# Kernel tuning notes

Hardware: AMD Instinct MI355X
Metric: run time of the kernel (lower is better)

The kernel has to match this reference:

```python
import jax, jax.numpy as jnp
import numpy as np

B = 16          # number of point clouds in the batch
N_COARSE = 1024 # coarse points per cloud
N_FINE = 4096   # fine (skip) points per cloud
C_IN = 256
C_SKIP = 128
K = 3
EPS = 1e-16


def setup_inputs() -> dict:
    key = jax.random.key(0)
    ks = jax.random.split(key, 8)
    x = jax.random.normal(ks[0], (B * N_COARSE, C_IN), dtype=jnp.float32)
    pos = jax.random.uniform(ks[1], (B * N_COARSE, 3), dtype=jnp.float32)
    x_skip = jax.random.normal(ks[2], (B * N_FINE, C_SKIP), dtype=jnp.float32)
    pos_skip = jax.random.uniform(ks[3], (B * N_FINE, 3), dtype=jnp.float32)
    batch = jnp.repeat(jnp.arange(B, dtype=jnp.int64), N_COARSE)
    batch_skip = jnp.repeat(jnp.arange(B, dtype=jnp.int64), N_FINE)
    W1 = jax.random.normal(ks[4], (C_IN + C_SKIP, 256), dtype=jnp.float32) * (1.0 / np.sqrt(C_IN + C_SKIP))
    b1 = jnp.zeros((256,), dtype=jnp.float32)
    W2 = jax.random.normal(ks[5], (256, 256), dtype=jnp.float32) * (1.0 / np.sqrt(256))
    b2 = jnp.zeros((256,), dtype=jnp.float32)
    return {"x": x, "pos": pos, "batch": batch, "x_skip": x_skip,
            "pos_skip": pos_skip, "batch_skip": batch_skip,
            "W1": W1, "b1": b1, "W2": W2, "b2": b2}


def _knn_interpolate(x, pos, pos_skip):
    # Equal-sized clouds: reshape to [B, N, *] and do batched kNN.
    xc = x.reshape(B, N_COARSE, C_IN)
    pc = pos.reshape(B, N_COARSE, 3)
    pf = pos_skip.reshape(B, N_FINE, 3)
    # squared pairwise distances [B, M, N]
    d2 = (jnp.sum(pf * pf, -1)[:, :, None]
          + jnp.sum(pc * pc, -1)[:, None, :]
          - 2.0 * jnp.einsum('bmd,bnd->bmn', pf, pc))
    d2 = jnp.maximum(d2, 0.0)
    neg_d2k, idx = jax.lax.top_k(-d2, K)          # k smallest distances
    w = 1.0 / jnp.maximum(-neg_d2k, EPS)          # [B, M, K] inverse-sq-dist weights
    gathered = jax.vmap(lambda f, i: f[i])(xc, idx)  # [B, M, K, C]
    y = jnp.sum(w[..., None] * gathered, axis=2) / jnp.sum(w, axis=2, keepdims=True)
    return y.reshape(B * N_FINE, C_IN)


def reference(x, pos, batch, x_skip, pos_skip, batch_skip, W1, b1, W2, b2):
    x_interp = _knn_interpolate(x, pos, pos_skip)          # [B*M, C_IN]
    h = jnp.concatenate([x_interp, x_skip], axis=1)        # [B*M, C_IN + C_SKIP]
    h = jax.nn.relu(h @ W1 + b1)
    out = jax.nn.relu(h @ W2 + b2)
    return out
```

## Files before the change

### kernel.cpp

```cpp
#include <hip/hip_runtime.h>

typedef float  f32x4  __attribute__((ext_vector_type(4)));
typedef short  short8 __attribute__((ext_vector_type(8)));
typedef unsigned short ushort_t;
typedef ushort_t us4   __attribute__((ext_vector_type(4)));

#define NCOARSE 1024
#define NFINE   4096

__device__ __forceinline__ ushort_t f2bf(float f){
  union { float f; unsigned u; } a; a.f = f;
  unsigned u = a.u;
  return (ushort_t)((u + 0x7fffu + ((u >> 16) & 1u)) >> 16);
}

__device__ __forceinline__ f32x4 splat4(float v){ f32x4 t = {v, v, v, v}; return t; }

__global__ void prep_w(const float* __restrict__ W, ushort_t* __restrict__ Wp, int nelem){
  int e = blockIdx.x * 256 + threadIdx.x;
  if (e >= nelem) return;
  int j    = e & 7;
  int lane = (e >> 3) & 63;
  int g    = e >> 9;
  int nb   = g & 15;
  int kc   = g >> 4;
  int k = kc * 32 + (lane >> 4) * 8 + j;
  int n = nb * 16 + (lane & 15);
  Wp[e] = f2bf(W[k * 256 + n]);
}

__global__ __launch_bounds__(256) void knn_kernel(const float* __restrict__ pos,
                           const float* __restrict__ pos_skip,
                           int* __restrict__ knn_i, float* __restrict__ knn_w){
  __shared__ f32x4 cand[8][129];
  const int tid = threadIdx.x;
  const int b   = blockIdx.x >> 6;
  const int mA  = blockIdx.x * 64 + (tid >> 3);
  const int mB  = mA + 32;
  const int chunk = tid & 7;

  const float* p = pos + (size_t)b * NCOARSE * 3;
  for (int c = tid; c < NCOARSE; c += 256){
    float x = p[3*c], y = p[3*c+1], z = p[3*c+2];
    float sc = __fadd_rn(__fadd_rn(__fmul_rn(x,x), __fmul_rn(y,y)), __fmul_rn(z,z));
    f32x4 v = { x, y, z, sc };
    cand[c >> 7][c & 127] = v;
  }
  __syncthreads();

  const float* qA = pos_skip + (size_t)mA * 3;
  const float* qB = pos_skip + (size_t)mB * 3;
  float ax = qA[0], ay = qA[1], az = qA[2];
  float bx = qB[0], by = qB[1], bz = qB[2];
  float sfA = __fadd_rn(__fadd_rn(__fmul_rn(ax,ax), __fmul_rn(ay,ay)), __fmul_rn(az,az));
  float sfB = __fadd_rn(__fadd_rn(__fmul_rn(bx,bx), __fmul_rn(by,by)), __fmul_rn(bz,bz));

  float dA0 = 1e30f, dA1 = 1e30f, dA2 = 1e30f;
  int   iA0 = 0,     iA1 = 0,     iA2 = 0;
  float dB0 = 1e30f, dB1 = 1e30f, dB2 = 1e30f;
  int   iB0 = 0,     iB1 = 0,     iB2 = 0;
  const int gbase = chunk * 128;
  #pragma unroll 2
  for (int i = 0; i < 128; ++i){
    f32x4 v = cand[chunk][i];
    int gi = gbase + i;
    float dotA = __fadd_rn(__fadd_rn(__fmul_rn(ax, v.x), __fmul_rn(ay, v.y)),
                           __fmul_rn(az, v.z));
    float dA = fmaxf(__fsub_rn(__fadd_rn(sfA, v.w), __fmul_rn(2.0f, dotA)), 0.0f);
    if (dA < dA2){
      if (dA < dA1){
        dA2 = dA1; iA2 = iA1;
        if (dA < dA0){ dA1 = dA0; iA1 = iA0; dA0 = dA; iA0 = gi; }
        else         { dA1 = dA;  iA1 = gi; }
      } else { dA2 = dA; iA2 = gi; }
    }
    float dotB = __fadd_rn(__fadd_rn(__fmul_rn(bx, v.x), __fmul_rn(by, v.y)),
                           __fmul_rn(bz, v.z));
    float dB = fmaxf(__fsub_rn(__fadd_rn(sfB, v.w), __fmul_rn(2.0f, dotB)), 0.0f);
    if (dB < dB2){
      if (dB < dB1){
        dB2 = dB1; iB2 = iB1;
        if (dB < dB0){ dB1 = dB0; iB1 = iB0; dB0 = dB; iB0 = gi; }
        else         { dB1 = dB;  iB1 = gi; }
      } else { dB2 = dB; iB2 = gi; }
    }
  }

  #pragma unroll
  for (int mlev = 1; mlev <= 4; mlev <<= 1){
    float e0 = __shfl_xor(dA0, mlev), e1 = __shfl_xor(dA1, mlev), e2 = __shfl_xor(dA2, mlev);
    int   j0 = __shfl_xor(iA0, mlev), j1 = __shfl_xor(iA1, mlev), j2 = __shfl_xor(iA2, mlev);
    #pragma unroll
    for (int s = 0; s < 3; ++s){
      float e = (s == 0) ? e0 : (s == 1) ? e1 : e2;
      int   j = (s == 0) ? j0 : (s == 1) ? j1 : j2;
      bool l2 = (e < dA2) || (e == dA2 && j < iA2);
      if (l2){
        bool l1 = (e < dA1) || (e == dA1 && j < iA1);
        if (l1){
          dA2 = dA1; iA2 = iA1;
          bool l0 = (e < dA0) || (e == dA0 && j < iA0);
          if (l0){ dA1 = dA0; iA1 = iA0; dA0 = e; iA0 = j; }
          else   { dA1 = e;  iA1 = j; }
        } else { dA2 = e; iA2 = j; }
      }
    }
    float f0 = __shfl_xor(dB0, mlev), f1 = __shfl_xor(dB1, mlev), f2 = __shfl_xor(dB2, mlev);
    int   k0 = __shfl_xor(iB0, mlev), k1 = __shfl_xor(iB1, mlev), k2 = __shfl_xor(iB2, mlev);
    #pragma unroll
    for (int s = 0; s < 3; ++s){
      float e = (s == 0) ? f0 : (s == 1) ? f1 : f2;
      int   j = (s == 0) ? k0 : (s == 1) ? k1 : k2;
      bool l2 = (e < dB2) || (e == dB2 && j < iB2);
      if (l2){
        bool l1 = (e < dB1) || (e == dB1 && j < iB1);
        if (l1){
          dB2 = dB1; iB2 = iB1;
          bool l0 = (e < dB0) || (e == dB0 && j < iB0);
          if (l0){ dB1 = dB0; iB1 = iB0; dB0 = e; iB0 = j; }
          else   { dB1 = e;  iB1 = j; }
        } else { dB2 = e; iB2 = j; }
      }
    }
  }

  if (chunk == 0){
    {
      float w0 = 1.0f / fmaxf(dA0, 1e-16f);
      float w1 = 1.0f / fmaxf(dA1, 1e-16f);
      float w2 = 1.0f / fmaxf(dA2, 1e-16f);
      float ws = __fadd_rn(__fadd_rn(w0, w1), w2);
      knn_i[3*mA]   = b * NCOARSE + iA0;
      knn_i[3*mA+1] = b * NCOARSE + iA1;
      knn_i[3*mA+2] = b * NCOARSE + iA2;
      knn_w[3*mA]   = w0 / ws;
      knn_w[3*mA+1] = w1 / ws;
      knn_w[3*mA+2] = w2 / ws;
    }
    {
      float w0 = 1.0f / fmaxf(dB0, 1e-16f);
      float w1 = 1.0f / fmaxf(dB1, 1e-16f);
      float w2 = 1.0f / fmaxf(dB2, 1e-16f);
      float ws = __fadd_rn(__fadd_rn(w0, w1), w2);
      knn_i[3*mB]   = b * NCOARSE + iB0;
      knn_i[3*mB+1] = b * NCOARSE + iB1;
      knn_i[3*mB+2] = b * NCOARSE + iB2;
      knn_w[3*mB]   = w0 / ws;
      knn_w[3*mB+1] = w1 / ws;
      knn_w[3*mB+2] = w2 / ws;
    }
  }
}

#define LDW4(DST, WP, STEP)                                                   \
  { _Pragma("unroll")                                                         \
    for (int n_ = 0; n_ < 4; ++n_)                                            \
      DST[n_] = *(const short8*)((WP) +                                       \
          ((size_t)(((STEP) * 16 + wp * 4 + n_) * 64 + lane)) * 8); }

__global__ __launch_bounds__(256, 3)
void fused_fp(const float* __restrict__ x, const float* __restrict__ x_skip,
              const int* __restrict__ knn_i, const float* __restrict__ knn_w,
              const ushort_t* __restrict__ W1p, const float* __restrict__ b1,
              const ushort_t* __restrict__ W2p, const float* __restrict__ b2,
              float* __restrict__ out){
  __shared__ ushort_t hbuf[32 * 384];
  char* h1b = (char*)hbuf;
  char* h2b = (char*)hbuf;
  const int tid  = threadIdx.x;
  const int lb   = ((blockIdx.x & 7) << 8) + (blockIdx.x >> 3);
  const int row0 = lb * 32;
  const int wp   = tid >> 6;
  const int lane = tid & 63;
  const int lhi  = lane >> 4;
  const int llo  = lane & 15;

  {
    const int r   = tid >> 3;
    const int sub = tid & 7;
    const int m   = row0 + r;
    const f32x4* xsr = (const f32x4*)(x_skip + (size_t)m * 128);
    f32x4 xs[4];
    #pragma unroll
    for (int it = 0; it < 4; ++it) xs[it] = xsr[it * 8 + sub];
    int i0 = knn_i[3*m], i1 = knn_i[3*m+1], i2 = knn_i[3*m+2];
    float w0 = knn_w[3*m], w1 = knn_w[3*m+1], w2 = knn_w[3*m+2];
    const f32x4* x0 = (const f32x4*)(x + (size_t)i0 * 256);
    const f32x4* x1 = (const f32x4*)(x + (size_t)i1 * 256);
    const f32x4* x2 = (const f32x4*)(x + (size_t)i2 * 256);
    #pragma unroll
    for (int it = 0; it < 8; ++it){
      int c4 = it * 8 + sub;
      f32x4 v = x0[c4] * w0 + x1[c4] * w1 + x2[c4] * w2;
      int byte = (r * 768 + c4 * 8) ^ ((r & 7) << 4);
      us4 pk = { f2bf(v.x), f2bf(v.y), f2bf(v.z), f2bf(v.w) };
      *(us4*)(h1b + byte) = pk;
    }
    #pragma unroll
    for (int it = 0; it < 4; ++it){
      int c4 = it * 8 + sub;
      f32x4 v = xs[it];
      int byte = (r * 768 + 512 + c4 * 8) ^ ((r & 7) << 4);
      us4 pk = { f2bf(v.x), f2bf(v.y), f2bf(v.z), f2bf(v.w) };
      *(us4*)(h1b + byte) = pk;
    }
  }
  __syncthreads();

  f32x4 acc[2][4];
  #pragma unroll
  for (int nbp = 0; nbp < 4; ++nbp){
    float bb = b1[wp * 64 + nbp * 16 + llo];
    #pragma unroll
    for (int mb = 0; mb < 2; ++mb) acc[mb][nbp] = splat4(bb);
  }
  {
    short8 wr[3][4];
    LDW4(wr[0], W1p, 0);
    LDW4(wr[1], W1p, 1);
    LDW4(wr[2], W1p, 2);
    #pragma unroll
    for (int kk = 0; kk < 12; ++kk){
      short8 af[2];
      #pragma unroll
      for (int mb = 0; mb < 2; ++mb){
        int rr = mb * 16 + llo;
        int byte = (rr * 768 + kk * 64 + lhi * 16) ^ ((rr & 7) << 4);
        af[mb] = *(const short8*)(h1b + byte);
      }
      #pragma unroll
      for (int mb = 0; mb < 2; ++mb)
        #pragma unroll
        for (int nbp = 0; nbp < 4; ++nbp)
          acc[mb][nbp] = __builtin_amdgcn_mfma_f32_16x16x32_bf16(
              af[mb], wr[kk % 3][nbp], acc[mb][nbp], 0, 0, 0);
      if (kk + 3 < 12) { LDW4(wr[kk % 3], W1p, kk + 3); }
    }
  }
  __syncthreads();

  #pragma unroll
  for (int mb = 0; mb < 2; ++mb)
    #pragma unroll
    for (int nbp = 0; nbp < 4; ++nbp)
      #pragma unroll
      for (int rg = 0; rg < 4; ++rg){
        int rr  = mb * 16 + lhi * 4 + rg;
        int col = wp * 64 + nbp * 16 + llo;
        int byte = (rr * 512 + col * 2) ^ ((rr & 7) << 4);
        *(ushort_t*)(h2b + byte) = f2bf(fmaxf(acc[mb][nbp][rg], 0.0f));
      }
  __syncthreads();

  f32x4 acc2[2][4];
  #pragma unroll
  for (int nbp = 0; nbp < 4; ++nbp){
    float bb = b2[wp * 64 + nbp * 16 + llo];
    #pragma unroll
    for (int mb = 0; mb < 2; ++mb) acc2[mb][nbp] = splat4(bb);
  }
  {
    short8 wr[3][4];
    LDW4(wr[0], W2p, 0);
    LDW4(wr[1], W2p, 1);
    LDW4(wr[2], W2p, 2);
    #pragma unroll
    for (int kk = 0; kk < 8; ++kk){
      short8 af[2];
      #pragma unroll
      for (int mb = 0; mb < 2; ++mb){
        int rr = mb * 16 + llo;
        int byte = (rr * 512 + kk * 64 + lhi * 16) ^ ((rr & 7) << 4);
        af[mb] = *(const short8*)(h2b + byte);
      }
      #pragma unroll
      for (int mb = 0; mb < 2; ++mb)
        #pragma unroll
        for (int nbp = 0; nbp < 4; ++nbp)
          acc2[mb][nbp] = __builtin_amdgcn_mfma_f32_16x16x32_bf16(
              af[mb], wr[kk % 3][nbp], acc2[mb][nbp], 0, 0, 0);
      if (kk + 3 < 8) { LDW4(wr[kk % 3], W2p, kk + 3); }
    }
  }

  #pragma unroll
  for (int mb = 0; mb < 2; ++mb)
    #pragma unroll
    for (int nbp = 0; nbp < 4; ++nbp)
      #pragma unroll
      for (int rg = 0; rg < 4; ++rg){
        int row = row0 + mb * 16 + lhi * 4 + rg;
        int col = wp * 64 + nbp * 16 + llo;
        out[(size_t)row * 256 + col] = fmaxf(acc2[mb][nbp][rg], 0.0f);
      }
}

extern "C" void kernel_launch(void* const* d_in, const int* in_sizes, int n_in,
                              void* d_out, int out_size, void* d_ws, size_t ws_size,
                              hipStream_t stream){
  (void)in_sizes; (void)n_in; (void)out_size; (void)ws_size;
  const float* x        = (const float*)d_in[0];
  const float* pos      = (const float*)d_in[1];
  const float* x_skip   = (const float*)d_in[3];
  const float* pos_skip = (const float*)d_in[4];
  const float* W1 = (const float*)d_in[6];
  const float* b1 = (const float*)d_in[7];
  const float* W2 = (const float*)d_in[8];
  const float* b2 = (const float*)d_in[9];
  float* out = (float*)d_out;
  char* ws = (char*)d_ws;
  ushort_t* W1p = (ushort_t*)(ws);
  ushort_t* W2p = (ushort_t*)(ws + 196608);
  int*      ki  = (int*)(ws + 327680);
  float*    kw  = (float*)(ws + 1114112);

  hipLaunchKernelGGL(prep_w, dim3(384), dim3(256), 0, stream, W1, W1p, 98304);
  hipLaunchKernelGGL(prep_w, dim3(256), dim3(256), 0, stream, W2, W2p, 65536);
  hipLaunchKernelGGL(knn_kernel, dim3(1024), dim3(256), 0, stream, pos, pos_skip, ki, kw);
  hipLaunchKernelGGL(fused_fp, dim3(2048), dim3(256), 0, stream,
                     x, x_skip, ki, kw, W1p, b1, W2p, b2, out);
}
```

Before: 93.10 us.

## Make fused MLP kernel persistent with register-resident weights and double-buffered gather

The fused MLP kernel becomes persistent: 256 blocks of 512 threads each process 8 tiles of 32 rows. All W1/W2 fragments are loaded into registers once per block instead of being streamed per tile. The kNN gather of the next tile into a second LDS buffer is issued while the second GEMM of the current tile runs, aiming to hide gather latency and cut repeated weight traffic. The cost is heavy register pressure (40 short8 weight fragments per thread at 2 waves/SIMD) and only 256 blocks, which may underfill the GPU. The weight loads use inline asm followed by an explicit vmcnt wait.

```diff
diff --git a/kernel.cpp b/kernel.cpp
--- a/kernel.cpp
+++ b/kernel.cpp
@@ -7,6 +7,9 @@
 
 #define NCOARSE 1024
 #define NFINE   4096
+
+#define GLD(dst, ptr) \
+  asm volatile("global_load_dwordx4 %0, %1, off" : "=&v"(dst) : "v"(ptr))
 
 __device__ __forceinline__ ushort_t f2bf(float f){
   union { float f; unsigned u; } a; a.f = f;
@@ -152,73 +155,84 @@
   }
 }
 
-#define LDW4(DST, WP, STEP)                                                   \
-  { _Pragma("unroll")                                                         \
-    for (int n_ = 0; n_ < 4; ++n_)                                            \
-      DST[n_] = *(const short8*)((WP) +                                       \
-          ((size_t)(((STEP) * 16 + wp * 4 + n_) * 64 + lane)) * 8); }
-
-__global__ __launch_bounds__(256, 3)
+__global__ __launch_bounds__(512, 2)
 void fused_fp(const float* __restrict__ x, const float* __restrict__ x_skip,
               const int* __restrict__ knn_i, const float* __restrict__ knn_w,
               const ushort_t* __restrict__ W1p, const float* __restrict__ b1,
               const ushort_t* __restrict__ W2p, const float* __restrict__ b2,
               float* __restrict__ out){
-  __shared__ ushort_t hbuf[32 * 384];
-  char* h1b = (char*)hbuf;
-  char* h2b = (char*)hbuf;
+  __shared__ ushort_t h1[2][32 * 384];
+  __shared__ ushort_t h2[32 * 256];
   const int tid  = threadIdx.x;
-  const int lb   = ((blockIdx.x & 7) << 8) + (blockIdx.x >> 3);
-  const int row0 = lb * 32;
-  const int wp   = tid >> 6;
+  const int lb   = ((blockIdx.x & 7) << 5) + (blockIdx.x >> 3);
+  const int wq   = tid >> 6;
   const int lane = tid & 63;
   const int lhi  = lane >> 4;
   const int llo  = lane & 15;
-
-  {
-    const int r   = tid >> 3;
-    const int sub = tid & 7;
-    const int m   = row0 + r;
-    const f32x4* xsr = (const f32x4*)(x_skip + (size_t)m * 128);
-    f32x4 xs[4];
-    #pragma unroll
-    for (int it = 0; it < 4; ++it) xs[it] = xsr[it * 8 + sub];
+  const int r    = tid >> 4;
+  const int sub  = tid & 15;
+
+  short8 w1f[12][2];
+  short8 w2f[8][2];
+  #pragma unroll
+  for (int kk = 0; kk < 12; ++kk)
+    #pragma unroll
+    for (int nb = 0; nb < 2; ++nb){
+      const ushort_t* p = W1p + ((size_t)((kk * 16 + wq * 2 + nb) * 64 + lane)) * 8;
+      GLD(w1f[kk][nb], p);
+    }
+  #pragma unroll
+  for (int kk = 0; kk < 8; ++kk)
+    #pragma unroll
+    for (int nb = 0; nb < 2; ++nb){
+      const ushort_t* p = W2p + ((size_t)((kk * 16 + wq * 2 + nb) * 64 + lane)) * 8;
+      GLD(w2f[kk][nb], p);
+    }
+
+  const float bb10 = b1[wq * 32 + llo];
+  const float bb11 = b1[wq * 32 + 16 + llo];
+  const float bb20 = b2[wq * 32 + llo];
+  const float bb21 = b2[wq * 32 + 16 + llo];
+
+  auto gather_tile = [&](char* h1b, int row0){
+    const int m = row0 + r;
     int i0 = knn_i[3*m], i1 = knn_i[3*m+1], i2 = knn_i[3*m+2];
     float w0 = knn_w[3*m], w1 = knn_w[3*m+1], w2 = knn_w[3*m+2];
     const f32x4* x0 = (const f32x4*)(x + (size_t)i0 * 256);
     const f32x4* x1 = (const f32x4*)(x + (size_t)i1 * 256);
     const f32x4* x2 = (const f32x4*)(x + (size_t)i2 * 256);
     #pragma unroll
-    for (int it = 0; it < 8; ++it){
-      int c4 = it * 8 + sub;
+    for (int it = 0; it < 4; ++it){
+      int c4 = it * 16 + sub;
       f32x4 v = x0[c4] * w0 + x1[c4] * w1 + x2[c4] * w2;
       int byte = (r * 768 + c4 * 8) ^ ((r & 7) << 4);
       us4 pk = { f2bf(v.x), f2bf(v.y), f2bf(v.z), f2bf(v.w) };
       *(us4*)(h1b + byte) = pk;
     }
-    #pragma unroll
-    for (int it = 0; it < 4; ++it){
-      int c4 = it * 8 + sub;
-      f32x4 v = xs[it];
+    const f32x4* xs = (const f32x4*)(x_skip + (size_t)m * 128);
+    #pragma unroll
+    for (int it = 0; it < 2; ++it){
+      int c4 = it * 16 + sub;
+      f32x4 v = xs[c4];
       int byte = (r * 768 + 512 + c4 * 8) ^ ((r & 7) << 4);
       us4 pk = { f2bf(v.x), f2bf(v.y), f2bf(v.z), f2bf(v.w) };
       *(us4*)(h1b + byte) = pk;
     }
-  }
+  };
+
+  gather_tile((char*)h1[0], lb * 256);
+  asm volatile("s_waitcnt vmcnt(0)");
+  __builtin_amdgcn_sched_barrier(0);
   __syncthreads();
 
-  f32x4 acc[2][4];
-  #pragma unroll
-  for (int nbp = 0; nbp < 4; ++nbp){
-    float bb = b1[wp * 64 + nbp * 16 + llo];
-    #pragma unroll
-    for (int mb = 0; mb < 2; ++mb) acc[mb][nbp] = splat4(bb);
-  }
-  {
-    short8 wr[3][4];
-    LDW4(wr[0], W1p, 0);
-    LDW4(wr[1], W1p, 1);
-    LDW4(wr[2], W1p, 2);
+  for (int t = 0; t < 8; ++t){
+    const int rowbase = lb * 256 + t * 32;
+    char* h1b = (char*)h1[t & 1];
+    char* h2b = (char*)h2;
+
+    f32x4 acc1[2][2];
+    acc1[0][0] = splat4(bb10); acc1[1][0] = splat4(bb10);
+    acc1[0][1] = splat4(bb11); acc1[1][1] = splat4(bb11);
     #pragma unroll
     for (int kk = 0; kk < 12; ++kk){
       short8 af[2];
@@ -231,39 +245,29 @@
       #pragma unroll
       for (int mb = 0; mb < 2; ++mb)
         #pragma unroll
-        for (int nbp = 0; nbp < 4; ++nbp)
-          acc[mb][nbp] = __builtin_amdgcn_mfma_f32_16x16x32_bf16(
-              af[mb], wr[kk % 3][nbp], acc[mb][nbp], 0, 0, 0);
-      if (kk + 3 < 12) { LDW4(wr[kk % 3], W1p, kk + 3); }
-    }
-  }
-  __syncthreads();
-
-  #pragma unroll
-  for (int mb = 0; mb < 2; ++mb)
-    #pragma unroll
-    for (int nbp = 0; nbp < 4; ++nbp)
-      #pragma unroll
-      for (int rg = 0; rg < 4; ++rg){
-        int rr  = mb * 16 + lhi * 4 + rg;
-        int col = wp * 64 + nbp * 16 + llo;
-        int byte = (rr * 512 + col * 2) ^ ((rr & 7) << 4);
-        *(ushort_t*)(h2b + byte) = f2bf(fmaxf(acc[mb][nbp][rg], 0.0f));
-      }
-  __syncthreads();
-
-  f32x4 acc2[2][4];
-  #pragma unroll
-  for (int nbp = 0; nbp < 4; ++nbp){
-    float bb = b2[wp * 64 + nbp * 16 + llo];
-    #pragma unroll
-    for (int mb = 0; mb < 2; ++mb) acc2[mb][nbp] = splat4(bb);
-  }
-  {
-    short8 wr[3][4];
-    LDW4(wr[0], W2p, 0);
-    LDW4(wr[1], W2p, 1);
-    LDW4(wr[2], W2p, 2);
+        for (int nb = 0; nb < 2; ++nb)
+          acc1[mb][nb] = __builtin_amdgcn_mfma_f32_16x16x32_bf16(
+              af[mb], w1f[kk][nb], acc1[mb][nb], 0, 0, 0);
+    }
+
+    #pragma unroll
+    for (int mb = 0; mb < 2; ++mb)
+      #pragma unroll
+      for (int nb = 0; nb < 2; ++nb)
+        #pragma unroll
+        for (int rg = 0; rg < 4; ++rg){
+          int rr  = mb * 16 + lhi * 4 + rg;
+          int col = wq * 32 + nb * 16 + llo;
+          int byte = (rr * 512 + col * 2) ^ ((rr & 7) << 4);
+          *(ushort_t*)(h2b + byte) = f2bf(fmaxf(acc1[mb][nb][rg], 0.0f));
+        }
+    __syncthreads();
+
+    if (t < 7) gather_tile((char*)h1[(t + 1) & 1], rowbase + 32);
+
+    f32x4 acc2[2][2];
+    acc2[0][0] = splat4(bb20); acc2[1][0] = splat4(bb20);
+    acc2[0][1] = splat4(bb21); acc2[1][1] = splat4(bb21);
     #pragma unroll
     for (int kk = 0; kk < 8; ++kk){
       short8 af[2];
@@ -276,23 +280,24 @@
       #pragma unroll
       for (int mb = 0; mb < 2; ++mb)
         #pragma unroll
-        for (int nbp = 0; nbp < 4; ++nbp)
-          acc2[mb][nbp] = __builtin_amdgcn_mfma_f32_16x16x32_bf16(
-              af[mb], wr[kk % 3][nbp], acc2[mb][nbp], 0, 0, 0);
-      if (kk + 3 < 8) { LDW4(wr[kk % 3], W2p, kk + 3); }
-    }
-  }
-
-  #pragma unroll
-  for (int mb = 0; mb < 2; ++mb)
-    #pragma unroll
-    for (int nbp = 0; nbp < 4; ++nbp)
-      #pragma unroll
-      for (int rg = 0; rg < 4; ++rg){
-        int row = row0 + mb * 16 + lhi * 4 + rg;
-        int col = wp * 64 + nbp * 16 + llo;
-        out[(size_t)row * 256 + col] = fmaxf(acc2[mb][nbp][rg], 0.0f);
-      }
+        for (int nb = 0; nb < 2; ++nb)
+          acc2[mb][nb] = __builtin_amdgcn_mfma_f32_16x16x32_bf16(
+              af[mb], w2f[kk][nb], acc2[mb][nb], 0, 0, 0);
+    }
+
+    #pragma unroll
+    for (int mb = 0; mb < 2; ++mb)
+      #pragma unroll
+      for (int nb = 0; nb < 2; ++nb)
+        #pragma unroll
+        for (int rg = 0; rg < 4; ++rg){
+          int row = rowbase + mb * 16 + lhi * 4 + rg;
+          int col = wq * 32 + nb * 16 + llo;
+          out[(size_t)row * 256 + col] = fmaxf(acc2[mb][nb][rg], 0.0f);
+        }
+
+    if (t < 7) __syncthreads();
+  }
 }
 
 extern "C" void kernel_launch(void* const* d_in, const int* in_sizes, int n_in,
@@ -317,6 +322,6 @@
   hipLaunchKernelGGL(prep_w, dim3(384), dim3(256), 0, stream, W1, W1p, 98304);
   hipLaunchKernelGGL(prep_w, dim3(256), dim3(256), 0, stream, W2, W2p, 65536);
   hipLaunchKernelGGL(knn_kernel, dim3(1024), dim3(256), 0, stream, pos, pos_skip, ki, kw);
-  hipLaunchKernelGGL(fused_fp, dim3(2048), dim3(256), 0, stream,
+  hipLaunchKernelGGL(fused_fp, dim3(256), dim3(512), 0, stream,
                      x, x_skip, ki, kw, W1p, b1, W2p, b2, out);
 }
```

Result: slower. 127.6 us (+37.1%).
